# Kernel tuning notes

Measured on AMD Instinct MI355X. Metric: run time of the kernel, lower is better.

The kernel has to match this reference:

```python
import jax, jax.numpy as jnp
import numpy as np

N = 4096      # nodes = mi_num + dis_num
IN = 4096     # in_size = mi_num + dis_num
H = 1024      # hidd_list = [H, H]
P = 256       # num_proj_hidden
TAU = 0.5
ALPHA = 0.8


def setup_inputs() -> dict:
    key = jax.random.key(0)
    ks = jax.random.split(key, 24)
    u = lambda k, shape, s: jax.random.uniform(k, shape, jnp.float32, -s, s)
    sH = 1.0 / np.sqrt(H)      # HGNN_conv stdv = 1/sqrt(out_ft)
    sP2 = 1.0 / np.sqrt(2 * P)
    sP = 1.0 / np.sqrt(P)
    inp = {
        "x1": jax.random.normal(ks[0], (N, IN), jnp.float32),
        "adj1": jax.random.uniform(ks[1], (N, N), jnp.float32) / N,  # normalized dense hypergraph Laplacian
        "x2": jax.random.normal(ks[2], (N, IN), jnp.float32),
        "adj2": jax.random.uniform(ks[3], (N, N), jnp.float32) / N,
        # hgcn1 (view 1) layers
        "W1a": u(ks[4], (IN, H), sH), "b1a": u(ks[5], (H,), sH),
        "W1b": u(ks[6], (H, H), sH),  "b1b": u(ks[7], (H,), sH),
        # hgcn2 (view 2) layers
        "W2a": u(ks[8], (IN, H), sH), "b2a": u(ks[9], (H,), sH),
        "W2b": u(ks[10], (H, H), sH), "b2b": u(ks[11], (H,), sH),
        # shared projection head (Linear stored as [in, out])
        "fc1_w": u(ks[12], (2 * H, H), sH),     "fc1_b": u(ks[13], (H,), sH),
        "fc11_w": u(ks[14], (H, 2 * P), sP2),   "fc11_b": u(ks[15], (2 * P,), sP2),
        "fc12_w": u(ks[16], (2 * P, P), sP),    "fc12_b": u(ks[17], (P,), sP),
        "fc2_w": u(ks[18], (P, 2 * P), sP2),    "fc2_b": u(ks[19], (2 * P,), sP2),
        "fc3_w": u(ks[20], (2 * P, P), sP),     "fc3_b": u(ks[21], (P,), sP),
    }
    return inp


def _hgcn(x, G, Wa, ba, Wb, bb):
    # HGNN_conv: G @ (x @ W + b), then leaky_relu(0.25); JumpingKnowledge 'cat'
    h1 = jax.nn.leaky_relu(G @ (x @ Wa + ba), 0.25)   # [N, H]
    h2 = jax.nn.leaky_relu(G @ (h1 @ Wb + bb), 0.25)  # [N, H]
    return jnp.concatenate([h1, h2], axis=1)          # [N, 2H]


def _projection(z, fc1_w, fc1_b, fc11_w, fc11_b, fc12_w, fc12_b, fc2_w, fc2_b, fc3_w, fc3_b):
    e = jax.nn.elu
    z = e(z @ fc1_w + fc1_b)
    z = e(z @ fc11_w + fc11_b)
    z = e(z @ fc12_w + fc12_b)
    z = e(z @ fc2_w + fc2_b)
    return z @ fc3_w + fc3_b  # [N, P]


def _sim(z1, z2):
    # InfoNCE-style loss; F.normalize with eps 1e-12
    n1 = z1 / jnp.maximum(jnp.linalg.norm(z1, axis=1, keepdims=True), 1e-12)
    n2 = z2 / jnp.maximum(jnp.linalg.norm(z2, axis=1, keepdims=True), 1e-12)
    refl = jnp.exp((n1 @ n1.T) / TAU)      # [N, N]
    between = jnp.exp((n1 @ n2.T) / TAU)   # [N, N]
    d_b = jnp.diagonal(between)
    d_r = jnp.diagonal(refl)
    loss = -jnp.log(d_b / (refl.sum(1) + between.sum(1) - d_r))
    # torch: loss.sum(dim=-1).mean() on a 1-D vector == scalar sum
    return loss.sum()


def reference(x1, adj1, x2, adj2,
              W1a, b1a, W1b, b1b, W2a, b2a, W2b, b2b,
              fc1_w, fc1_b, fc11_w, fc11_b, fc12_w, fc12_b,
              fc2_w, fc2_b, fc3_w, fc3_b):
    z1 = _hgcn(x1, adj1, W1a, b1a, W1b, b1b)
    z2 = _hgcn(x2, adj2, W2a, b2a, W2b, b2b)
    proj = lambda z: _projection(z, fc1_w, fc1_b, fc11_w, fc11_b, fc12_w, fc12_b, fc2_w, fc2_b, fc3_w, fc3_b)
    h1 = proj(z1)
    h2 = proj(z2)
    loss = ALPHA * _sim(h1, h2) + (1.0 - ALPHA) * _sim(h2, h1)
    return (z1, z2, loss)
```

## Files before the change

kernel.cpp:

```cpp
#include <hip/hip_runtime.h>
#include <hip/hip_bf16.h>
#include <cstdint>

using bf16 = __hip_bfloat16;
typedef __attribute__((ext_vector_type(8))) short short8;
typedef __attribute__((ext_vector_type(4))) short short4v;
typedef __attribute__((ext_vector_type(4))) float floatx4;

#define DEVINL __device__ __forceinline__

DEVINL short bfbits(float v) { return __builtin_bit_cast(short, __float2bfloat16(v)); }

template<int ACT> DEVINL float activate(float v) {
  if constexpr (ACT == 1) return v > 0.f ? v : 0.25f * v;
  else if constexpr (ACT == 2) return v > 0.f ? v : __expf(v) - 1.f;
  else return v;
}

template<int ACT, int TRANS, int BIAS, int AF32, int OF32, int DUAL>
__global__ __launch_bounds__(256, 2)
void gemm_bt(const void* __restrict__ A1, const void* __restrict__ A2, int lda,
             const bf16* __restrict__ B1, const bf16* __restrict__ B2, int ldb,
             const float* __restrict__ bias1, const float* __restrict__ bias2,
             void* __restrict__ out1, void* __restrict__ out2,
             bf16* __restrict__ outB1, bf16* __restrict__ outB2,
             int ldo, int K)
{
  const int vz = blockIdx.z;
  const void* A = vz ? A2 : A1;
  const bf16* B = vz ? B2 : B1;
  const float* bias = vz ? bias2 : bias1;
  void* out = vz ? out2 : out1;
  bf16* outB = vz ? outB2 : outB1;

  __shared__ bf16 At[128 * 64];
  __shared__ bf16 Bt[128 * 64];
  const int t = threadIdx.x;
  const int wave = t >> 6, lane = t & 63;
  const int mBase = blockIdx.y * 128, nBase = blockIdx.x * 128;
  const int wm = (wave >> 1) * 64, wn = (wave & 1) * 64;
  const int q = lane >> 4, lm = lane & 15;

  floatx4 acc[4][4];
#pragma unroll
  for (int i = 0; i < 4; i++)
#pragma unroll
    for (int j = 0; j < 4; j++) acc[i][j] = (floatx4){0.f, 0.f, 0.f, 0.f};

  floatx4 apl[4], aph[4];
  short8  apb[4];
  short8  bpb[4];

  auto LA = [&](int kb) {
#pragma unroll
    for (int i = 0; i < 4; i++) {
      int c = i * 256 + t;
      size_t off = (size_t)(mBase + (c >> 3)) * lda + kb + ((c & 7) << 3);
      if constexpr (AF32) {
        const float* f = (const float*)A + off;
        apl[i] = *(const floatx4*)f;
        aph[i] = *(const floatx4*)(f + 4);
      } else {
        apb[i] = *(const short8*)((const bf16*)A + off);
      }
    }
  };
  auto LB = [&](int kb) {
#pragma unroll
    for (int i = 0; i < 4; i++) {
      int c = i * 256 + t;
      bpb[i] = *(const short8*)(B + (size_t)(nBase + (c >> 3)) * ldb + kb + ((c & 7) << 3));
    }
  };

  LA(0); LB(0);
  for (int kb = 0; kb < K; kb += 64) {
    __syncthreads();
#pragma unroll
    for (int i = 0; i < 4; i++) {
      int c = i * 256 + t;
      short8 r;
      if constexpr (AF32) {
#pragma unroll
        for (int j = 0; j < 4; j++) { r[j] = bfbits(apl[i][j]); r[4 + j] = bfbits(aph[i][j]); }
      } else {
        r = apb[i];
      }
      *(short8*)&At[c * 8] = r;
      *(short8*)&Bt[c * 8] = bpb[i];
    }
    __syncthreads();
    if (kb + 64 < K) { LA(kb + 64); LB(kb + 64); }
#pragma unroll
    for (int ks = 0; ks < 64; ks += 32) {
      short8 af[4], bfr[4];
#pragma unroll
      for (int i = 0; i < 4; i++)
        af[i] = *(const short8*)&At[(wm + i * 16 + lm) * 64 + ks + q * 8];
#pragma unroll
      for (int j = 0; j < 4; j++)
        bfr[j] = *(const short8*)&Bt[(wn + j * 16 + lm) * 64 + ks + q * 8];
#pragma unroll
      for (int i = 0; i < 4; i++)
#pragma unroll
        for (int j = 0; j < 4; j++)
          acc[i][j] = __builtin_amdgcn_mfma_f32_16x16x32_bf16(af[i], bfr[j], acc[i][j], 0, 0, 0);
    }
  }

#pragma unroll
  for (int i = 0; i < 4; i++) {
#pragma unroll
    for (int j = 0; j < 4; j++) {
      const int col = nBase + wn + j * 16 + lm;
      float bv2 = 0.f;
      if constexpr (BIAS) bv2 = bias[col];
      if constexpr (TRANS) {
        short4v pk;
#pragma unroll
        for (int r = 0; r < 4; r++)
          pk[r] = bfbits(activate<ACT>(acc[i][j][r] + bv2));
        const int row = mBase + wm + i * 16 + q * 4;
        *(short4v*)&((bf16*)out)[(size_t)col * ldo + row] = pk;
      } else {
#pragma unroll
        for (int r = 0; r < 4; r++) {
          const int row = mBase + wm + i * 16 + q * 4 + r;
          float v = activate<ACT>(acc[i][j][r] + bv2);
          if constexpr (OF32) ((float*)out)[(size_t)row * ldo + col] = v;
          else ((bf16*)out)[(size_t)row * ldo + col] = __float2bfloat16(v);
          if constexpr (DUAL) outB[(size_t)row * ldo + col] = __float2bfloat16(v);
        }
      }
    }
  }
}

__global__ __launch_bounds__(256, 2)
void sim3(const bf16* __restrict__ n1, const bf16* __restrict__ n2,
          float* __restrict__ R11, float* __restrict__ R22,
          float* __restrict__ R12, float* __restrict__ C12)
{
  const bf16 *A, *B; float *Rs, *Cs;
  if (blockIdx.z == 0)      { A = n1; B = n1; Rs = R11; Cs = nullptr; }
  else if (blockIdx.z == 1) { A = n2; B = n2; Rs = R22; Cs = nullptr; }
  else                      { A = n1; B = n2; Rs = R12; Cs = C12; }

  __shared__ bf16 At[128 * 64];
  __shared__ bf16 Bt[128 * 64];
  const int t = threadIdx.x;
  const int wave = t >> 6, lane = t & 63;
  const int mBase = blockIdx.y * 128, nBase = blockIdx.x * 128;
  const int wm = (wave >> 1) * 64, wn = (wave & 1) * 64;
  const int q = lane >> 4, lm = lane & 15;

  floatx4 acc[4][4];
#pragma unroll
  for (int i = 0; i < 4; i++)
#pragma unroll
    for (int j = 0; j < 4; j++) acc[i][j] = (floatx4){0.f, 0.f, 0.f, 0.f};

  short8 apb[4], bpb[4];
  auto LD = [&](int kb) {
#pragma unroll
    for (int i = 0; i < 4; i++) {
      int c = i * 256 + t;
      apb[i] = *(const short8*)(A + (size_t)(mBase + (c >> 3)) * 256 + kb + ((c & 7) << 3));
      bpb[i] = *(const short8*)(B + (size_t)(nBase + (c >> 3)) * 256 + kb + ((c & 7) << 3));
    }
  };

  LD(0);
  for (int kb = 0; kb < 256; kb += 64) {
    __syncthreads();
#pragma unroll
    for (int i = 0; i < 4; i++) {
      int c = i * 256 + t;
      *(short8*)&At[c * 8] = apb[i];
      *(short8*)&Bt[c * 8] = bpb[i];
    }
    __syncthreads();
    if (kb + 64 < 256) LD(kb + 64);
#pragma unroll
    for (int ks = 0; ks < 64; ks += 32) {
      short8 af[4], bfr[4];
#pragma unroll
      for (int i = 0; i < 4; i++)
        af[i] = *(const short8*)&At[(wm + i * 16 + lm) * 64 + ks + q * 8];
#pragma unroll
      for (int j = 0; j < 4; j++)
        bfr[j] = *(const short8*)&Bt[(wn + j * 16 + lm) * 64 + ks + q * 8];
#pragma unroll
      for (int i = 0; i < 4; i++)
#pragma unroll
        for (int j = 0; j < 4; j++)
          acc[i][j] = __builtin_amdgcn_mfma_f32_16x16x32_bf16(af[i], bfr[j], acc[i][j], 0, 0, 0);
    }
  }

  float rs[4][4], cs[4];
#pragma unroll
  for (int i = 0; i < 4; i++) { cs[i] = 0.f;
#pragma unroll
    for (int r = 0; r < 4; r++) rs[i][r] = 0.f; }

#pragma unroll
  for (int i = 0; i < 4; i++)
#pragma unroll
    for (int j = 0; j < 4; j++)
#pragma unroll
      for (int r = 0; r < 4; r++) {
        float e = __expf(2.f * acc[i][j][r]);
        rs[i][r] += e;
        cs[j] += e;
      }

#pragma unroll
  for (int i = 0; i < 4; i++)
#pragma unroll
    for (int r = 0; r < 4; r++) {
      float v = rs[i][r];
      v += __shfl_xor(v, 1); v += __shfl_xor(v, 2);
      v += __shfl_xor(v, 4); v += __shfl_xor(v, 8);
      if (lm == 0) atomicAdd(&Rs[mBase + wm + i * 16 + q * 4 + r], v);
    }
  if (Cs) {
#pragma unroll
    for (int j = 0; j < 4; j++) {
      float v = cs[j];
      v += __shfl_xor(v, 16); v += __shfl_xor(v, 32);
      if (lane < 16) atomicAdd(&Cs[nBase + wn + j * 16 + lane], v);
    }
  }
}

__global__ void transpose2_f32_bf16(const float* __restrict__ in1, const float* __restrict__ in2,
                                    bf16* __restrict__ out1, bf16* __restrict__ out2, int R, int C)
{
  const float* in = blockIdx.z ? in2 : in1;
  bf16* out = blockIdx.z ? out2 : out1;
  __shared__ float tile[32][33];
  const int bx = blockIdx.x * 32;
  const int by = blockIdx.y * 32;
  const int tx = threadIdx.x & 31, ty = threadIdx.x >> 5;
#pragma unroll
  for (int s = 0; s < 4; s++) {
    int r = ty + s * 8;
    tile[r][tx] = in[(size_t)(by + r) * C + bx + tx];
  }
  __syncthreads();
#pragma unroll
  for (int s = 0; s < 4; s++) {
    int r = ty + s * 8;
    out[(size_t)(bx + r) * R + by + tx] = __float2bfloat16(tile[tx][r]);
  }
}

__global__ void zero_f32(float* __restrict__ p, int n)
{
  int i = blockIdx.x * blockDim.x + threadIdx.x;
  if (i < n) p[i] = 0.f;
}

__global__ void norm_rows2(const bf16* __restrict__ h1, const bf16* __restrict__ h2,
                           bf16* __restrict__ o1, bf16* __restrict__ o2)
{
  const bf16* h = blockIdx.z ? h2 : h1;
  bf16* o = blockIdx.z ? o2 : o1;
  const int row = blockIdx.x * 4 + (threadIdx.x >> 6);
  const int lane = threadIdx.x & 63;
  float v[4]; float ss = 0.f;
#pragma unroll
  for (int j = 0; j < 4; j++) {
    v[j] = __bfloat162float(h[(size_t)row * 256 + lane * 4 + j]);
    ss += v[j] * v[j];
  }
  for (int m = 1; m < 64; m <<= 1) ss += __shfl_xor(ss, m);
  const float s = 1.0f / fmaxf(sqrtf(ss), 1e-12f);
#pragma unroll
  for (int j = 0; j < 4; j++)
    o[(size_t)row * 256 + lane * 4 + j] = __float2bfloat16(v[j] * s);
}

__global__ void loss_partial(const bf16* __restrict__ n1, const bf16* __restrict__ n2,
                             const float* __restrict__ R11, const float* __restrict__ R12,
                             const float* __restrict__ R22, const float* __restrict__ C12,
                             float* __restrict__ lossAcc)
{
  const int row = blockIdx.x * 4 + (threadIdx.x >> 6);
  const int lane = threadIdx.x & 63;
  float d12 = 0.f, d11 = 0.f, d22 = 0.f;
#pragma unroll
  for (int j = 0; j < 4; j++) {
    float a = __bfloat162float(n1[(size_t)row * 256 + lane * 4 + j]);
    float b = __bfloat162float(n2[(size_t)row * 256 + lane * 4 + j]);
    d12 += a * b; d11 += a * a; d22 += b * b;
  }
  for (int m = 1; m < 64; m <<= 1) {
    d12 += __shfl_xor(d12, m); d11 += __shfl_xor(d11, m); d22 += __shfl_xor(d22, m);
  }
  if (lane == 0) {
    float a1 = fmaxf(R11[row] + R12[row] - __expf(2.f * d11), 1e-20f);
    float a2 = fmaxf(R22[row] + C12[row] - __expf(2.f * d22), 1e-20f);
    float l1 = logf(a1) - 2.f * d12;
    float l2 = logf(a2) - 2.f * d12;
    atomicAdd(lossAcc, 0.8f * l1 + 0.2f * l2);
  }
}

__global__ void finalize_loss(const float* __restrict__ lossAcc, float* __restrict__ out)
{
  if (threadIdx.x == 0) out[0] = *lossAcc;
}

extern "C" void kernel_launch(void* const* d_in, const int* in_sizes, int n_in,
                              void* d_out, int out_size, void* d_ws, size_t ws_size,
                              hipStream_t stream)
{
  (void)in_sizes; (void)n_in; (void)out_size; (void)ws_size;
  const float* x1   = (const float*)d_in[0];
  const float* adj1 = (const float*)d_in[1];
  const float* x2   = (const float*)d_in[2];
  const float* adj2 = (const float*)d_in[3];
  const float* W1a  = (const float*)d_in[4];  const float* b1a = (const float*)d_in[5];
  const float* W1b  = (const float*)d_in[6];  const float* b1b = (const float*)d_in[7];
  const float* W2a  = (const float*)d_in[8];  const float* b2a = (const float*)d_in[9];
  const float* W2b  = (const float*)d_in[10]; const float* b2b = (const float*)d_in[11];
  const float* fc1w = (const float*)d_in[12]; const float* fc1b = (const float*)d_in[13];
  const float* fc11w= (const float*)d_in[14]; const float* fc11b= (const float*)d_in[15];
  const float* fc12w= (const float*)d_in[16]; const float* fc12b= (const float*)d_in[17];
  const float* fc2w = (const float*)d_in[18]; const float* fc2b = (const float*)d_in[19];
  const float* fc3w = (const float*)d_in[20]; const float* fc3b = (const float*)d_in[21];

  float* z1 = (float*)d_out;
  float* z2 = z1 + (size_t)4096 * 2048;
  float* lossOut = z1 + (size_t)2 * 4096 * 2048;

  const size_t MB = 1u << 20;
  char* w = (char*)d_ws;
  bf16* WT1  = (bf16*)(w);
  bf16* WT2  = (bf16*)(w + 8 * MB);
  bf16* TT1  = (bf16*)(w + 16 * MB);
  bf16* TT2  = (bf16*)(w + 24 * MB);
  bf16* zB1  = (bf16*)(w + 32 * MB);
  bf16* zB2  = (bf16*)(w + 48 * MB);
  bf16* fc1T = (bf16*)(w + 64 * MB);
  bf16* fc11T= (bf16*)(w + 68 * MB);
  bf16* fc12T= (bf16*)(w + 69 * MB);
  bf16* fc2T = (bf16*)(w + 69 * MB + 256 * 1024);
  bf16* fc3T = (bf16*)(w + 69 * MB + 512 * 1024);
  float* R11 = (float*)(w + 69 * MB + 768 * 1024);
  float* R12 = R11 + 4096;
  float* R22 = R12 + 4096;
  float* C12 = R22 + 4096;
  float* lossAcc = C12 + 4096;
  bf16* P1_1 = (bf16*)(w);
  bf16* P1_2 = (bf16*)(w + 8 * MB);
  bf16* P2_1 = (bf16*)(w + 16 * MB);
  bf16* P2_2 = (bf16*)(w + 20 * MB);
  bf16* P3_1 = (bf16*)(w + 24 * MB);
  bf16* P3_2 = (bf16*)(w + 26 * MB);
  bf16* P4_1 = (bf16*)(w + 28 * MB);
  bf16* P4_2 = (bf16*)(w);
  bf16* Hp1  = (bf16*)(w + 4 * MB);
  bf16* Hp2  = (bf16*)(w + 6 * MB);
  bf16* n1   = (bf16*)(w + 8 * MB);
  bf16* n2   = (bf16*)(w + 10 * MB);

  dim3 blk(256);

  zero_f32<<<dim3(65), blk, 0, stream>>>(R11, 4 * 4096 + 1);

  transpose2_f32_bf16<<<dim3(32, 64, 1), blk, 0, stream>>>(fc1w, fc1w, fc1T, fc1T, 2048, 1024);
  transpose2_f32_bf16<<<dim3(16, 32, 1), blk, 0, stream>>>(fc11w, fc11w, fc11T, fc11T, 1024, 512);
  transpose2_f32_bf16<<<dim3(8, 16, 1),  blk, 0, stream>>>(fc12w, fc12w, fc12T, fc12T, 512, 256);
  transpose2_f32_bf16<<<dim3(16, 8, 1),  blk, 0, stream>>>(fc2w, fc2w, fc2T, fc2T, 256, 512);
  transpose2_f32_bf16<<<dim3(8, 16, 1),  blk, 0, stream>>>(fc3w, fc3w, fc3T, fc3T, 512, 256);

  transpose2_f32_bf16<<<dim3(32, 128, 2), blk, 0, stream>>>(W1a, W2a, WT1, WT2, 4096, 1024);
  gemm_bt<0, 1, 1, 1, 0, 0><<<dim3(8, 32, 2), blk, 0, stream>>>(
      x1, x2, 4096, WT1, WT2, 4096, b1a, b2a, TT1, TT2, nullptr, nullptr, 4096, 4096);
  gemm_bt<1, 0, 0, 1, 1, 1><<<dim3(8, 32, 2), blk, 0, stream>>>(
      adj1, adj2, 4096, TT1, TT2, 4096, nullptr, nullptr, z1, z2, zB1, zB2, 2048, 4096);
  transpose2_f32_bf16<<<dim3(32, 32, 2), blk, 0, stream>>>(W1b, W2b, WT1, WT2, 1024, 1024);
  gemm_bt<0, 1, 1, 0, 0, 0><<<dim3(8, 32, 2), blk, 0, stream>>>(
      zB1, zB2, 2048, WT1, WT2, 1024, b1b, b2b, TT1, TT2, nullptr, nullptr, 4096, 1024);
  gemm_bt<1, 0, 0, 1, 1, 1><<<dim3(8, 32, 2), blk, 0, stream>>>(
      adj1, adj2, 4096, TT1, TT2, 4096, nullptr, nullptr, z1 + 1024, z2 + 1024, zB1 + 1024, zB2 + 1024, 2048, 4096);

  gemm_bt<2, 0, 1, 0, 0, 0><<<dim3(8, 32, 2), blk, 0, stream>>>(
      zB1, zB2, 2048, fc1T, fc1T, 2048, fc1b, fc1b, P1_1, P1_2, nullptr, nullptr, 1024, 2048);
  gemm_bt<2, 0, 1, 0, 0, 0><<<dim3(4, 32, 2), blk, 0, stream>>>(
      P1_1, P1_2, 1024, fc11T, fc11T, 1024, fc11b, fc11b, P2_1, P2_2, nullptr, nullptr, 512, 1024);
  gemm_bt<2, 0, 1, 0, 0, 0><<<dim3(2, 32, 2), blk, 0, stream>>>(
      P2_1, P2_2, 512, fc12T, fc12T, 512, fc12b, fc12b, P3_1, P3_2, nullptr, nullptr, 256, 512);
  gemm_bt<2, 0, 1, 0, 0, 0><<<dim3(4, 32, 2), blk, 0, stream>>>(
      P3_1, P3_2, 256, fc2T, fc2T, 256, fc2b, fc2b, P4_1, P4_2, nullptr, nullptr, 512, 256);
  gemm_bt<0, 0, 1, 0, 0, 0><<<dim3(2, 32, 2), blk, 0, stream>>>(
      P4_1, P4_2, 512, fc3T, fc3T, 512, fc3b, fc3b, Hp1, Hp2, nullptr, nullptr, 256, 512);
  norm_rows2<<<dim3(1024, 1, 2), blk, 0, stream>>>(Hp1, Hp2, n1, n2);

  sim3<<<dim3(32, 32, 3), blk, 0, stream>>>(n1, n2, R11, R22, R12, C12);

  loss_partial<<<dim3(1024), blk, 0, stream>>>(n1, n2, R11, R12, R22, C12, lossAcc);
  finalize_loss<<<dim3(1), dim3(64), 0, stream>>>(lossAcc, lossOut);
}
```

Baseline: 982.0 us.

## Pre-convert adj and x to bf16 and stream GEMM tiles via direct-to-LDS loads

Adds a pass that converts adj and x from fp32 to bf16 once, reusing the adj copy across both propagation GEMMs. The bf16 GEMM path now loads global memory straight into double-buffered LDS with global_load_lds, which removes the register staging and one barrier per k-step. Workgroup ids are remapped so consecutive blocks spread across the 8 XCDs. The converted copies need about 200 MB of workspace and an extra conversion pass, and the code falls back to the fp32 path when the workspace is smaller.

```diff
diff --git a/kernel.cpp b/kernel.cpp
--- a/kernel.cpp
+++ b/kernel.cpp
@@ -10,6 +10,11 @@
 #define DEVINL __device__ __forceinline__
 
 DEVINL short bfbits(float v) { return __builtin_bit_cast(short, __float2bfloat16(v)); }
+
+DEVINL void gload_lds16(const void* g, void* l) {
+  __builtin_amdgcn_global_load_lds((const __attribute__((address_space(1))) void*)g,
+                                   (__attribute__((address_space(3))) void*)l, 16, 0, 0);
+}
 
 template<int ACT> DEVINL float activate(float v) {
   if constexpr (ACT == 1) return v > 0.f ? v : 0.25f * v;
@@ -26,12 +31,165 @@
              bf16* __restrict__ outB1, bf16* __restrict__ outB2,
              int ldo, int K)
 {
-  const int vz = blockIdx.z;
+  const int gx = gridDim.x, gy = gridDim.y;
+  const int nwg = gx * gy * gridDim.z;
+  int bx, by, vz;
+  if (nwg & 7) {
+    bx = blockIdx.x; by = blockIdx.y; vz = blockIdx.z;
+  } else {
+    const int flat = blockIdx.x + gx * (blockIdx.y + gy * blockIdx.z);
+    const int cpx = nwg >> 3;
+    const int w = (flat & 7) * cpx + (flat >> 3);
+    bx = w % gx;
+    const int tmp = w / gx;
+    by = tmp % gy;
+    vz = tmp / gy;
+  }
+
   const void* A = vz ? A2 : A1;
   const bf16* B = vz ? B2 : B1;
   const float* bias = vz ? bias2 : bias1;
   void* out = vz ? out2 : out1;
   bf16* outB = vz ? outB2 : outB1;
+
+  constexpr int NBUF = AF32 ? 1 : 2;
+  __shared__ bf16 At[NBUF][128 * 64];
+  __shared__ bf16 Bt[NBUF][128 * 64];
+  const int t = threadIdx.x;
+  const int wave = t >> 6, lane = t & 63;
+  const int mBase = by * 128, nBase = bx * 128;
+  const int wm = (wave >> 1) * 64, wn = (wave & 1) * 64;
+  const int q = lane >> 4, lm = lane & 15;
+
+  floatx4 acc[4][4];
+#pragma unroll
+  for (int i = 0; i < 4; i++)
+#pragma unroll
+    for (int j = 0; j < 4; j++) acc[i][j] = (floatx4){0.f, 0.f, 0.f, 0.f};
+
+  if constexpr (!AF32) {
+    auto STAGE = [&](int buf, int kb) {
+#pragma unroll
+      for (int i = 0; i < 4; i++) {
+        const int c0 = i * 256 + wave * 64;
+        const int c = c0 + lane;
+        const bf16* ga = (const bf16*)A + (size_t)(mBase + (c >> 3)) * lda + kb + ((c & 7) << 3);
+        const bf16* gb = B + (size_t)(nBase + (c >> 3)) * ldb + kb + ((c & 7) << 3);
+        gload_lds16(ga, &At[buf][c0 * 8]);
+        gload_lds16(gb, &Bt[buf][c0 * 8]);
+      }
+    };
+    int cur = 0;
+    STAGE(0, 0);
+    for (int kb = 0; kb < K; kb += 64) {
+      __syncthreads();
+      if (kb + 64 < K) STAGE(cur ^ 1, kb + 64);
+#pragma unroll
+      for (int ks = 0; ks < 64; ks += 32) {
+        short8 af[4], bfr[4];
+#pragma unroll
+        for (int i = 0; i < 4; i++)
+          af[i] = *(const short8*)&At[cur][(wm + i * 16 + lm) * 64 + ks + q * 8];
+#pragma unroll
+        for (int j = 0; j < 4; j++)
+          bfr[j] = *(const short8*)&Bt[cur][(wn + j * 16 + lm) * 64 + ks + q * 8];
+#pragma unroll
+        for (int i = 0; i < 4; i++)
+#pragma unroll
+          for (int j = 0; j < 4; j++)
+            acc[i][j] = __builtin_amdgcn_mfma_f32_16x16x32_bf16(af[i], bfr[j], acc[i][j], 0, 0, 0);
+      }
+      cur ^= 1;
+    }
+  } else {
+    floatx4 apl[4], aph[4];
+    short8 bpb[4];
+    auto LA = [&](int kb) {
+#pragma unroll
+      for (int i = 0; i < 4; i++) {
+        int c = i * 256 + t;
+        size_t off = (size_t)(mBase + (c >> 3)) * lda + kb + ((c & 7) << 3);
+        const float* f = (const float*)A + off;
+        apl[i] = *(const floatx4*)f;
+        aph[i] = *(const floatx4*)(f + 4);
+      }
+    };
+    auto LB = [&](int kb) {
+#pragma unroll
+      for (int i = 0; i < 4; i++) {
+        int c = i * 256 + t;
+        bpb[i] = *(const short8*)(B + (size_t)(nBase + (c >> 3)) * ldb + kb + ((c & 7) << 3));
+      }
+    };
+    LA(0); LB(0);
+    for (int kb = 0; kb < K; kb += 64) {
+      __syncthreads();
+#pragma unroll
+      for (int i = 0; i < 4; i++) {
+        int c = i * 256 + t;
+        short8 r;
+#pragma unroll
+        for (int j = 0; j < 4; j++) { r[j] = bfbits(apl[i][j]); r[4 + j] = bfbits(aph[i][j]); }
+        *(short8*)&At[0][c * 8] = r;
+        *(short8*)&Bt[0][c * 8] = bpb[i];
+      }
+      __syncthreads();
+      if (kb + 64 < K) { LA(kb + 64); LB(kb + 64); }
+#pragma unroll
+      for (int ks = 0; ks < 64; ks += 32) {
+        short8 af[4], bfr[4];
+#pragma unroll
+        for (int i = 0; i < 4; i++)
+          af[i] = *(const short8*)&At[0][(wm + i * 16 + lm) * 64 + ks + q * 8];
+#pragma unroll
+        for (int j = 0; j < 4; j++)
+          bfr[j] = *(const short8*)&Bt[0][(wn + j * 16 + lm) * 64 + ks + q * 8];
+#pragma unroll
+        for (int i = 0; i < 4; i++)
+#pragma unroll
+          for (int j = 0; j < 4; j++)
+            acc[i][j] = __builtin_amdgcn_mfma_f32_16x16x32_bf16(af[i], bfr[j], acc[i][j], 0, 0, 0);
+      }
+    }
+  }
+
+#pragma unroll
+  for (int i = 0; i < 4; i++) {
+#pragma unroll
+    for (int j = 0; j < 4; j++) {
+      const int col = nBase + wn + j * 16 + lm;
+      float bv2 = 0.f;
+      if constexpr (BIAS) bv2 = bias[col];
+      if constexpr (TRANS) {
+        short4v pk;
+#pragma unroll
+        for (int r = 0; r < 4; r++)
+          pk[r] = bfbits(activate<ACT>(acc[i][j][r] + bv2));
+        const int row = mBase + wm + i * 16 + q * 4;
+        *(short4v*)&((bf16*)out)[(size_t)col * ldo + row] = pk;
+      } else {
+#pragma unroll
+        for (int r = 0; r < 4; r++) {
+          const int row = mBase + wm + i * 16 + q * 4 + r;
+          float v = activate<ACT>(acc[i][j][r] + bv2);
+          if constexpr (OF32) ((float*)out)[(size_t)row * ldo + col] = v;
+          else ((bf16*)out)[(size_t)row * ldo + col] = __float2bfloat16(v);
+          if constexpr (DUAL) outB[(size_t)row * ldo + col] = __float2bfloat16(v);
+        }
+      }
+    }
+  }
+}
+
+__global__ __launch_bounds__(256, 2)
+void sim3(const bf16* __restrict__ n1, const bf16* __restrict__ n2,
+          float* __restrict__ R11, float* __restrict__ R22,
+          float* __restrict__ R12, float* __restrict__ C12)
+{
+  const bf16 *A, *B; float *Rs, *Cs;
+  if (blockIdx.z == 0)      { A = n1; B = n1; Rs = R11; Cs = nullptr; }
+  else if (blockIdx.z == 1) { A = n2; B = n2; Rs = R22; Cs = nullptr; }
+  else                      { A = n1; B = n2; Rs = R12; Cs = C12; }
 
   __shared__ bf16 At[128 * 64];
   __shared__ bf16 Bt[128 * 64];
@@ -47,119 +205,6 @@
 #pragma unroll
     for (int j = 0; j < 4; j++) acc[i][j] = (floatx4){0.f, 0.f, 0.f, 0.f};
 
-  floatx4 apl[4], aph[4];
-  short8  apb[4];
-  short8  bpb[4];
-
-  auto LA = [&](int kb) {
-#pragma unroll
-    for (int i = 0; i < 4; i++) {
-      int c = i * 256 + t;
-      size_t off = (size_t)(mBase + (c >> 3)) * lda + kb + ((c & 7) << 3);
-      if constexpr (AF32) {
-        const float* f = (const float*)A + off;
-        apl[i] = *(const floatx4*)f;
-        aph[i] = *(const floatx4*)(f + 4);
-      } else {
-        apb[i] = *(const short8*)((const bf16*)A + off);
-      }
-    }
-  };
-  auto LB = [&](int kb) {
-#pragma unroll
-    for (int i = 0; i < 4; i++) {
-      int c = i * 256 + t;
-      bpb[i] = *(const short8*)(B + (size_t)(nBase + (c >> 3)) * ldb + kb + ((c & 7) << 3));
-    }
-  };
-
-  LA(0); LB(0);
-  for (int kb = 0; kb < K; kb += 64) {
-    __syncthreads();
-#pragma unroll
-    for (int i = 0; i < 4; i++) {
-      int c = i * 256 + t;
-      short8 r;
-      if constexpr (AF32) {
-#pragma unroll
-        for (int j = 0; j < 4; j++) { r[j] = bfbits(apl[i][j]); r[4 + j] = bfbits(aph[i][j]); }
-      } else {
-        r = apb[i];
-      }
-      *(short8*)&At[c * 8] = r;
-      *(short8*)&Bt[c * 8] = bpb[i];
-    }
-    __syncthreads();
-    if (kb + 64 < K) { LA(kb + 64); LB(kb + 64); }
-#pragma unroll
-    for (int ks = 0; ks < 64; ks += 32) {
-      short8 af[4], bfr[4];
-#pragma unroll
-      for (int i = 0; i < 4; i++)
-        af[i] = *(const short8*)&At[(wm + i * 16 + lm) * 64 + ks + q * 8];
-#pragma unroll
-      for (int j = 0; j < 4; j++)
-        bfr[j] = *(const short8*)&Bt[(wn + j * 16 + lm) * 64 + ks + q * 8];
-#pragma unroll
-      for (int i = 0; i < 4; i++)
-#pragma unroll
-        for (int j = 0; j < 4; j++)
-          acc[i][j] = __builtin_amdgcn_mfma_f32_16x16x32_bf16(af[i], bfr[j], acc[i][j], 0, 0, 0);
-    }
-  }
-
-#pragma unroll
-  for (int i = 0; i < 4; i++) {
-#pragma unroll
-    for (int j = 0; j < 4; j++) {
-      const int col = nBase + wn + j * 16 + lm;
-      float bv2 = 0.f;
-      if constexpr (BIAS) bv2 = bias[col];
-      if constexpr (TRANS) {
-        short4v pk;
-#pragma unroll
-        for (int r = 0; r < 4; r++)
-          pk[r] = bfbits(activate<ACT>(acc[i][j][r] + bv2));
-        const int row = mBase + wm + i * 16 + q * 4;
-        *(short4v*)&((bf16*)out)[(size_t)col * ldo + row] = pk;
-      } else {
-#pragma unroll
-        for (int r = 0; r < 4; r++) {
-          const int row = mBase + wm + i * 16 + q * 4 + r;
-          float v = activate<ACT>(acc[i][j][r] + bv2);
-          if constexpr (OF32) ((float*)out)[(size_t)row * ldo + col] = v;
-          else ((bf16*)out)[(size_t)row * ldo + col] = __float2bfloat16(v);
-          if constexpr (DUAL) outB[(size_t)row * ldo + col] = __float2bfloat16(v);
-        }
-      }
-    }
-  }
-}
-
-__global__ __launch_bounds__(256, 2)
-void sim3(const bf16* __restrict__ n1, const bf16* __restrict__ n2,
-          float* __restrict__ R11, float* __restrict__ R22,
-          float* __restrict__ R12, float* __restrict__ C12)
-{
-  const bf16 *A, *B; float *Rs, *Cs;
-  if (blockIdx.z == 0)      { A = n1; B = n1; Rs = R11; Cs = nullptr; }
-  else if (blockIdx.z == 1) { A = n2; B = n2; Rs = R22; Cs = nullptr; }
-  else                      { A = n1; B = n2; Rs = R12; Cs = C12; }
-
-  __shared__ bf16 At[128 * 64];
-  __shared__ bf16 Bt[128 * 64];
-  const int t = threadIdx.x;
-  const int wave = t >> 6, lane = t & 63;
-  const int mBase = blockIdx.y * 128, nBase = blockIdx.x * 128;
-  const int wm = (wave >> 1) * 64, wn = (wave & 1) * 64;
-  const int q = lane >> 4, lm = lane & 15;
-
-  floatx4 acc[4][4];
-#pragma unroll
-  for (int i = 0; i < 4; i++)
-#pragma unroll
-    for (int j = 0; j < 4; j++) acc[i][j] = (floatx4){0.f, 0.f, 0.f, 0.f};
-
   short8 apb[4], bpb[4];
   auto LD = [&](int kb) {
 #pragma unroll
@@ -256,6 +301,22 @@
   }
 }
 
+__global__ void convert2_f32_bf16(const float* __restrict__ in1, const float* __restrict__ in2,
+                                  bf16* __restrict__ out1, bf16* __restrict__ out2, int n8)
+{
+  const float* in = blockIdx.z ? in2 : in1;
+  bf16* out = blockIdx.z ? out2 : out1;
+  const int i = blockIdx.x * 256 + threadIdx.x;
+  if (i >= n8) return;
+  const size_t off = (size_t)i * 8;
+  floatx4 a = *(const floatx4*)(in + off);
+  floatx4 b = *(const floatx4*)(in + off + 4);
+  short8 r;
+#pragma unroll
+  for (int j = 0; j < 4; j++) { r[j] = bfbits(a[j]); r[4 + j] = bfbits(b[j]); }
+  *(short8*)(out + off) = r;
+}
+
 __global__ void zero_f32(float* __restrict__ p, int n)
 {
   int i = blockIdx.x * blockDim.x + threadIdx.x;
@@ -317,7 +378,7 @@
                               void* d_out, int out_size, void* d_ws, size_t ws_size,
                               hipStream_t stream)
 {
-  (void)in_sizes; (void)n_in; (void)out_size; (void)ws_size;
+  (void)in_sizes; (void)n_in; (void)out_size;
   const float* x1   = (const float*)d_in[0];
   const float* adj1 = (const float*)d_in[1];
   const float* x2   = (const float*)d_in[2];
@@ -366,10 +427,21 @@
   bf16* Hp2  = (bf16*)(w + 6 * MB);
   bf16* n1   = (bf16*)(w + 8 * MB);
   bf16* n2   = (bf16*)(w + 10 * MB);
+  bf16* adjB1 = (bf16*)(w + 72 * MB);
+  bf16* adjB2 = (bf16*)(w + 104 * MB);
+  bf16* xB1   = (bf16*)(w + 136 * MB);
+  bf16* xB2   = (bf16*)(w + 168 * MB);
+  const bool cvtAdj = ws_size >= 136 * MB;
+  const bool cvtX   = ws_size >= 200 * MB;
 
   dim3 blk(256);
 
   zero_f32<<<dim3(65), blk, 0, stream>>>(R11, 4 * 4096 + 1);
+
+  if (cvtAdj)
+    convert2_f32_bf16<<<dim3(8192, 1, 2), blk, 0, stream>>>(adj1, adj2, adjB1, adjB2, 2097152);
+  if (cvtX)
+    convert2_f32_bf16<<<dim3(8192, 1, 2), blk, 0, stream>>>(x1, x2, xB1, xB2, 2097152);
 
   transpose2_f32_bf16<<<dim3(32, 64, 1), blk, 0, stream>>>(fc1w, fc1w, fc1T, fc1T, 2048, 1024);
   transpose2_f32_bf16<<<dim3(16, 32, 1), blk, 0, stream>>>(fc11w, fc11w, fc11T, fc11T, 1024, 512);
@@ -378,15 +450,27 @@
   transpose2_f32_bf16<<<dim3(8, 16, 1),  blk, 0, stream>>>(fc3w, fc3w, fc3T, fc3T, 512, 256);
 
   transpose2_f32_bf16<<<dim3(32, 128, 2), blk, 0, stream>>>(W1a, W2a, WT1, WT2, 4096, 1024);
-  gemm_bt<0, 1, 1, 1, 0, 0><<<dim3(8, 32, 2), blk, 0, stream>>>(
-      x1, x2, 4096, WT1, WT2, 4096, b1a, b2a, TT1, TT2, nullptr, nullptr, 4096, 4096);
-  gemm_bt<1, 0, 0, 1, 1, 1><<<dim3(8, 32, 2), blk, 0, stream>>>(
-      adj1, adj2, 4096, TT1, TT2, 4096, nullptr, nullptr, z1, z2, zB1, zB2, 2048, 4096);
+  if (cvtX)
+    gemm_bt<0, 1, 1, 0, 0, 0><<<dim3(8, 32, 2), blk, 0, stream>>>(
+        xB1, xB2, 4096, WT1, WT2, 4096, b1a, b2a, TT1, TT2, nullptr, nullptr, 4096, 4096);
+  else
+    gemm_bt<0, 1, 1, 1, 0, 0><<<dim3(8, 32, 2), blk, 0, stream>>>(
+        x1, x2, 4096, WT1, WT2, 4096, b1a, b2a, TT1, TT2, nullptr, nullptr, 4096, 4096);
+  if (cvtAdj)
+    gemm_bt<1, 0, 0, 0, 1, 1><<<dim3(8, 32, 2), blk, 0, stream>>>(
+        adjB1, adjB2, 4096, TT1, TT2, 4096, nullptr, nullptr, z1, z2, zB1, zB2, 2048, 4096);
+  else
+    gemm_bt<1, 0, 0, 1, 1, 1><<<dim3(8, 32, 2), blk, 0, stream>>>(
+        adj1, adj2, 4096, TT1, TT2, 4096, nullptr, nullptr, z1, z2, zB1, zB2, 2048, 4096);
   transpose2_f32_bf16<<<dim3(32, 32, 2), blk, 0, stream>>>(W1b, W2b, WT1, WT2, 1024, 1024);
   gemm_bt<0, 1, 1, 0, 0, 0><<<dim3(8, 32, 2), blk, 0, stream>>>(
       zB1, zB2, 2048, WT1, WT2, 1024, b1b, b2b, TT1, TT2, nullptr, nullptr, 4096, 1024);
-  gemm_bt<1, 0, 0, 1, 1, 1><<<dim3(8, 32, 2), blk, 0, stream>>>(
-      adj1, adj2, 4096, TT1, TT2, 4096, nullptr, nullptr, z1 + 1024, z2 + 1024, zB1 + 1024, zB2 + 1024, 2048, 4096);
+  if (cvtAdj)
+    gemm_bt<1, 0, 0, 0, 1, 1><<<dim3(8, 32, 2), blk, 0, stream>>>(
+        adjB1, adjB2, 4096, TT1, TT2, 4096, nullptr, nullptr, z1 + 1024, z2 + 1024, zB1 + 1024, zB2 + 1024, 2048, 4096);
+  else
+    gemm_bt<1, 0, 0, 1, 1, 1><<<dim3(8, 32, 2), blk, 0, stream>>>(
+        adj1, adj2, 4096, TT1, TT2, 4096, nullptr, nullptr, z1 + 1024, z2 + 1024, zB1 + 1024, zB2 + 1024, 2048, 4096);
 
   gemm_bt<2, 0, 1, 0, 0, 0><<<dim3(8, 32, 2), blk, 0, stream>>>(
       zB1, zB2, 2048, fc1T, fc1T, 2048, fc1b, fc1b, P1_1, P1_2, nullptr, nullptr, 1024, 2048);
```

Result: faster. 939.8 us (-4.3%).
